# Optimization experiments

Hardware: AMD Instinct MI355X
Metric: run time of the kernel (lower is better)

Reference implementation:

```python
import jax, jax.numpy as jnp
import numpy as np

NEG_SLOPE = 0.01  # torch nn.LeakyReLU default


def _lrelu(x):
    return jax.nn.leaky_relu(x, NEG_SLOPE)


def _conv1x1(x, w):
    # x: [B,C,H,W], w: [O,C] -> [B,O,H,W]  (1x1 conv, no bias)
    return jnp.einsum('bchw,oc->bohw', x, w)


def _distance_matrix(scale, H, W, dtype):
    # even-scale branch of the torch code
    x = jnp.arange(-(scale // 2), scale // 2 + 1, dtype=dtype)  # len scale+1
    x = jnp.concatenate([x[: (scale + 1) // 2], x[(scale + 1) // 2 + 1:]])  # drop middle -> len scale
    d0 = jnp.broadcast_to(x[None, :], (scale, scale))
    d1 = d0.T
    d2 = jnp.sqrt(d0 ** 2 + d1 ** 2)
    dm = jnp.stack([d0, d1, d2], axis=0)            # [3, s, s]
    dm = jnp.tile(dm, (1, H // scale, W // scale))   # [3, H, W]
    return dm[None]                                  # [1, 3, H, W]


def setup_inputs() -> dict:
    key = jax.random.key(0)
    ks = jax.random.split(key, 10)
    B, C, h, w, scale = 1, 16, 256, 256, 4
    H, W = h * scale, w * scale
    f32 = jnp.float32

    def kaiming(k, shape):
        fan_out = shape[0]
        std = np.sqrt(2.0 / fan_out)
        return (jax.random.normal(k, shape, dtype=f32) * std)

    return {
        'lr_feature': jax.random.normal(ks[0], (B, C, h, w), dtype=f32),
        'hr_feature': jax.random.normal(ks[1], (B, C, H, W), dtype=f32),
        'w0': kaiming(ks[2], (32, 64)),
        'w1': kaiming(ks[3], (16, 32)),
        'w2': kaiming(ks[4], (8, 16)),
        'w3': kaiming(ks[5], (1, 8)),
        's0': kaiming(ks[6], (3, 3)),
        's1': kaiming(ks[7], (2, 3)),
        's2': kaiming(ks[8], (1, 2)),
        'wf': jnp.abs(kaiming(ks[9], (1, 2))),
    }


def reference(lr_feature, hr_feature, w0, w1, w2, w3, s0, s1, s2, wf):
    B, C, h, w = lr_feature.shape
    H, W = hr_feature.shape[-2:]
    scale = W // w  # static under jit

    # nearest-neighbor expand of lr_feature to hr resolution
    lr_up = jnp.repeat(jnp.repeat(lr_feature, scale, axis=2), scale, axis=3)

    # representation: [B, 4C, H, W]
    rep = jnp.concatenate(
        [lr_up, hr_feature, lr_up * hr_feature, (lr_up - hr_feature) ** 2], axis=1)

    # similarity_measure1: 4C->32->16->8->1, leaky relu after each
    o = _lrelu(_conv1x1(rep, w0))
    o = _lrelu(_conv1x1(o, w1))
    o = _lrelu(_conv1x1(o, w2))
    weights1 = _lrelu(_conv1x1(o, w3))  # [B,1,H,W]

    # similarity_measure2 on the tiled distance matrix: 3->3->2->1
    dm = _distance_matrix(scale, H, W, lr_feature.dtype)  # [1,3,H,W]
    o2 = _lrelu(_conv1x1(dm, s0))
    o2 = _lrelu(_conv1x1(o2, s1))
    weights2 = _lrelu(_conv1x1(o2, s2))  # [1,1,H,W]

    # fuse with abs-constrained weights
    fused_in = jnp.concatenate([weights1, weights2], axis=1)  # [B,2,H,W] (B=1)
    mapping = _lrelu(_conv1x1(fused_in, jnp.abs(wf)))
    return mapping
```

## Files before the change

### kernel.cpp

```cpp
#include <hip/hip_runtime.h>
#include <hip/hip_bf16.h>


typedef __attribute__((ext_vector_type(8))) short bf16x8;
typedef __attribute__((ext_vector_type(4))) short s16x4;
typedef __attribute__((ext_vector_type(4))) float f32x4;

union B8 { bf16x8 v; short2 p[4]; int d[4]; };
union B4 { s16x4 v; short2 p[2]; int d[2]; };

__device__ __forceinline__ float lrelu(float x) { return fmaxf(x, 0.01f * x); }

__device__ __forceinline__ short2 cvt2(float a, float b) {
    __hip_bfloat162 h = __float22bfloat162_rn(make_float2(a, b));
    short2 s; __builtin_memcpy(&s, &h, 4); return s;
}

__global__ __launch_bounds__(256) void ctx_mfma(
    const float* __restrict__ lr,  const float* __restrict__ hr,
    const float* __restrict__ w0g, const float* __restrict__ w1g,
    const float* __restrict__ w2g, const float* __restrict__ w3g,
    const float* __restrict__ s0g, const float* __restrict__ s1g,
    const float* __restrict__ s2g, const float* __restrict__ wfg,
    float* __restrict__ out)
{
    constexpr int W = 1024, HW = 1024 * 1024, LHW = 256 * 256;

    const int tid  = threadIdx.x;
    const int lane = tid & 63;
    const int g    = lane >> 4;
    const int px   = lane & 15;

    const int wave_id = blockIdx.x * 4 + (tid >> 6);
    const int y  = wave_id >> 3;
    const int xw = (wave_id & 7) << 7;

    B8 a1[2][2];
    #pragma unroll
    for (int m = 0; m < 2; ++m)
        #pragma unroll
        for (int q = 0; q < 2; ++q) {
            const float* wp = w0g + (m * 16 + px) * 64 + q * 32 + g * 8;
            #pragma unroll
            for (int j = 0; j < 4; ++j) a1[m][q].p[j] = cvt2(wp[2 * j], wp[2 * j + 1]);
        }
    B8 a2;
    {
        const float* wp = w1g + px * 32 + g * 8;
        #pragma unroll
        for (int j = 0; j < 4; ++j) a2.p[j] = cvt2(wp[2 * j], wp[2 * j + 1]);
    }
    B8 a3;
    {
        const bool val = (px < 8) && (g < 2);
        const float* wp = w2g + (px & 7) * 16 + (g & 1) * 8;
        const short2 z2s = make_short2(0, 0);
        #pragma unroll
        for (int j = 0; j < 4; ++j) a3.p[j] = val ? cvt2(wp[2 * j], wp[2 * j + 1]) : z2s;
    }
    const float4 w3v = *(const float4*)(w3g + (g & 1) * 4);

    const int xi = px & 3, yi = y & 3;
    const float d0 = (float)xi + ((xi < 2) ? -2.f : -1.f);
    const float d1 = (float)yi + ((yi < 2) ? -2.f : -1.f);
    const float d2 = sqrtf(d0 * d0 + d1 * d1);
    const float q0 = lrelu(s0g[0] * d0 + s0g[1] * d1 + s0g[2] * d2);
    const float q1 = lrelu(s0g[3] * d0 + s0g[4] * d1 + s0g[5] * d2);
    const float q2 = lrelu(s0g[6] * d0 + s0g[7] * d1 + s0g[8] * d2);
    const float u0 = lrelu(s1g[0] * q0 + s1g[1] * q1 + s1g[2] * q2);
    const float u1 = lrelu(s1g[3] * q0 + s1g[4] * q1 + s1g[5] * q2);
    const float wt2 = lrelu(s2g[0] * u0 + s2g[1] * u1);
    const float awf0 = fabsf(wfg[0]), awf1 = fabsf(wfg[1]);

    const int s0l = px + 16 * ((2 * g) & 3);
    const int s1l = s0l + 16;
    const bool glo = (g < 2);

    const int cb = (g & 1) << 3;
    int hr_idx[8], lr_idx[8];
    #pragma unroll
    for (int j = 0; j < 8; ++j) {
        hr_idx[j] = (cb + j) * HW  + y * W + xw + px;
        lr_idx[j] = (cb + j) * LHW + (y >> 2) * 256 + (xw >> 2) + (px >> 2);
    }
    const int oidx = y * W + xw + px;
    const f32x4 zf = {0.f, 0.f, 0.f, 0.f};

#define LOADT(LV, HV, T)                                                      \
    {                                                                         \
        _Pragma("unroll")                                                     \
        for (int j = 0; j < 8; ++j) {                                         \
            HV[j] = hr[hr_idx[j] + (T) * 16];                                 \
            LV[j] = lr[lr_idx[j] + (T) * 4];                                  \
        }                                                                     \
    }

#define COMPUTE(LV, HV, T)                                                    \
    {                                                                         \
        B8 b0, b1;                                                            \
        _Pragma("unroll")                                                     \
        for (int j = 0; j < 4; ++j) {                                         \
            float ua = glo ? LV[2 * j]     : HV[2 * j];                       \
            float ub = glo ? LV[2 * j + 1] : HV[2 * j + 1];                   \
            b0.p[j] = cvt2(ua, ub);                                           \
            float da = LV[2 * j]     - HV[2 * j];                             \
            float db = LV[2 * j + 1] - HV[2 * j + 1];                         \
            float pa = glo ? LV[2 * j]     * HV[2 * j]     : da * da;         \
            float pb = glo ? LV[2 * j + 1] * HV[2 * j + 1] : db * db;         \
            b1.p[j] = cvt2(pa, pb);                                           \
        }                                                                     \
        f32x4 acc1a = __builtin_amdgcn_mfma_f32_16x16x32_bf16(a1[0][0].v, b0.v, zf, 0, 0, 0); \
        acc1a = __builtin_amdgcn_mfma_f32_16x16x32_bf16(a1[0][1].v, b1.v, acc1a, 0, 0, 0);    \
        f32x4 acc1b = __builtin_amdgcn_mfma_f32_16x16x32_bf16(a1[1][0].v, b0.v, zf, 0, 0, 0); \
        acc1b = __builtin_amdgcn_mfma_f32_16x16x32_bf16(a1[1][1].v, b1.v, acc1b, 0, 0, 0);    \
        B4 za, zq;                                                            \
        za.p[0] = cvt2(lrelu(acc1a.x), lrelu(acc1a.y));                       \
        za.p[1] = cvt2(lrelu(acc1a.z), lrelu(acc1a.w));                       \
        zq.p[0] = cvt2(lrelu(acc1b.x), lrelu(acc1b.y));                       \
        zq.p[1] = cvt2(lrelu(acc1b.z), lrelu(acc1b.w));                       \
                   \
        int A0 = __shfl(za.d[0], s0l, 64);                                    \
        int A1 = __shfl(za.d[1], s0l, 64);                                    \
        int A2 = __shfl(za.d[0], s1l, 64);                                    \
        int A3 = __shfl(za.d[1], s1l, 64);                                    \
        int Q0 = __shfl(zq.d[0], s0l, 64);                                    \
        int Q1 = __shfl(zq.d[1], s0l, 64);                                    \
        int Q2 = __shfl(zq.d[0], s1l, 64);                                    \
        int Q3 = __shfl(zq.d[1], s1l, 64);                                    \
        B8 b2;                                                                \
        b2.d[0] = glo ? A0 : Q0;                                              \
        b2.d[1] = glo ? A1 : Q1;                                              \
        b2.d[2] = glo ? A2 : Q2;                                              \
        b2.d[3] = glo ? A3 : Q3;                                              \
        f32x4 acc2 = __builtin_amdgcn_mfma_f32_16x16x32_bf16(a2.v, b2.v, zf, 0, 0, 0); \
        B4 z2q;                                                               \
        z2q.p[0] = cvt2(lrelu(acc2.x), lrelu(acc2.y));                        \
        z2q.p[1] = cvt2(lrelu(acc2.z), lrelu(acc2.w));                        \
               \
        B8 b3;                                                                \
        b3.d[0] = __shfl(z2q.d[0], s0l, 64);                                  \
        b3.d[1] = __shfl(z2q.d[1], s0l, 64);                                  \
        b3.d[2] = __shfl(z2q.d[0], s1l, 64);                                  \
        b3.d[3] = __shfl(z2q.d[1], s1l, 64);                                  \
        f32x4 acc3 = __builtin_amdgcn_mfma_f32_16x16x32_bf16(a3.v, b3.v, zf, 0, 0, 0); \
        float part = w3v.x * lrelu(acc3.x) + w3v.y * lrelu(acc3.y)            \
                   + w3v.z * lrelu(acc3.z) + w3v.w * lrelu(acc3.w);           \
        float sum = part + __shfl_xor(part, 16, 64);                          \
        float wt1 = lrelu(sum);                                               \
        float res = lrelu(awf0 * wt1 + awf1 * wt2);                           \
        if (g == 0) out[oidx + (T) * 16] = res;                               \
    }

    float la[8], ha[8], lb[8], hb[8];
    LOADT(la, ha, 0);
    #pragma unroll
    for (int tt = 0; tt < 8; tt += 2) {
        LOADT(lb, hb, tt + 1);
        COMPUTE(la, ha, tt);
        if (tt + 2 < 8) LOADT(la, ha, tt + 2);
        COMPUTE(lb, hb, tt + 1);
    }
#undef LOADT
#undef COMPUTE
}

extern "C" void kernel_launch(void* const* d_in, const int* in_sizes, int n_in,
                              void* d_out, int out_size, void* d_ws, size_t ws_size,
                              hipStream_t stream) {
    const float* lr = (const float*)d_in[0];
    const float* hr = (const float*)d_in[1];
    const float* w0 = (const float*)d_in[2];
    const float* w1 = (const float*)d_in[3];
    const float* w2 = (const float*)d_in[4];
    const float* w3 = (const float*)d_in[5];
    const float* s0 = (const float*)d_in[6];
    const float* s1 = (const float*)d_in[7];
    const float* s2 = (const float*)d_in[8];
    const float* wf = (const float*)d_in[9];
    float* o = (float*)d_out;

    ctx_mfma<<<2048, 256, 0, stream>>>(lr, hr, w0, w1, w2, w3, s0, s1, s2, wf, o);
}
```

Baseline: 139.4 us.

## Stage inputs via direct global-to-LDS loads with triple-buffered pipeline

Each wave now copies its hr and lr input tiles straight into per-wave LDS with 16-byte global_load_lds transfers. These copies are triple-buffered and paced by manual vmcnt waits, instead of using per-lane scalar register loads with double buffering. The aim is to keep more memory requests in flight and issue wider loads for this latency-limited streaming kernel. The cost is extra LDS reads per tile, plus reliance on hand-counted vmcnt values that must match the issued load count exactly.

```diff
diff --git a/kernel.cpp b/kernel.cpp
--- a/kernel.cpp
+++ b/kernel.cpp
@@ -16,6 +16,12 @@
     short2 s; __builtin_memcpy(&s, &h, 4); return s;
 }
 
+__device__ __forceinline__ void gl16(const float* g, float* l) {
+    __builtin_amdgcn_global_load_lds(
+        (const __attribute__((address_space(1))) void*)g,
+        (__attribute__((address_space(3))) void*)l, 16, 0, 0);
+}
+
 __global__ __launch_bounds__(256) void ctx_mfma(
     const float* __restrict__ lr,  const float* __restrict__ hr,
     const float* __restrict__ w0g, const float* __restrict__ w1g,
@@ -26,12 +32,16 @@
 {
     constexpr int W = 1024, HW = 1024 * 1024, LHW = 256 * 256;
 
+    __shared__ __align__(16) float shr[4][3][16][16];
+    __shared__ __align__(16) float slr[4][3][16][4];
+
     const int tid  = threadIdx.x;
     const int lane = tid & 63;
+    const int widx = tid >> 6;
     const int g    = lane >> 4;
     const int px   = lane & 15;
 
-    const int wave_id = blockIdx.x * 4 + (tid >> 6);
+    const int wave_id = blockIdx.x * 4 + widx;
     const int y  = wave_id >> 3;
     const int xw = (wave_id & 7) << 7;
 
@@ -75,38 +85,38 @@
     const int s0l = px + 16 * ((2 * g) & 3);
     const int s1l = s0l + 16;
     const bool glo = (g < 2);
+    const int cb = (g & 1) << 3;
 
-    const int cb = (g & 1) << 3;
-    int hr_idx[8], lr_idx[8];
-    #pragma unroll
-    for (int j = 0; j < 8; ++j) {
-        hr_idx[j] = (cb + j) * HW  + y * W + xw + px;
-        lr_idx[j] = (cb + j) * LHW + (y >> 2) * 256 + (xw >> 2) + (px >> 2);
-    }
+    const float* hrs = hr + (lane >> 2) * HW + y * W + xw + (lane & 3) * 4;
+    const float* lrs = lr + (lane & 15) * LHW + (y >> 2) * 256 + (xw >> 2);
+
     const int oidx = y * W + xw + px;
     const f32x4 zf = {0.f, 0.f, 0.f, 0.f};
 
-#define LOADT(LV, HV, T)                                                      \
+#define STAGE(BUF, T)                                                         \
     {                                                                         \
+        gl16(hrs + (T) * 16, &shr[widx][BUF][0][0]);                          \
+        if (lane < 16) gl16(lrs + (T) * 4, &slr[widx][BUF][0][0]);            \
+    }
+
+#define COMP(BUF, T)                                                          \
+    {                                                                         \
+        float lrv[8], hrv[8];                                                 \
         _Pragma("unroll")                                                     \
         for (int j = 0; j < 8; ++j) {                                         \
-            HV[j] = hr[hr_idx[j] + (T) * 16];                                 \
-            LV[j] = lr[lr_idx[j] + (T) * 4];                                  \
+            hrv[j] = shr[widx][BUF][cb + j][px];                              \
+            lrv[j] = slr[widx][BUF][cb + j][px >> 2];                         \
         }                                                                     \
-    }
-
-#define COMPUTE(LV, HV, T)                                                    \
-    {                                                                         \
         B8 b0, b1;                                                            \
         _Pragma("unroll")                                                     \
         for (int j = 0; j < 4; ++j) {                                         \
-            float ua = glo ? LV[2 * j]     : HV[2 * j];                       \
-            float ub = glo ? LV[2 * j + 1] : HV[2 * j + 1];                   \
+            float ua = glo ? lrv[2 * j]     : hrv[2 * j];                     \
+            float ub = glo ? lrv[2 * j + 1] : hrv[2 * j + 1];                 \
             b0.p[j] = cvt2(ua, ub);                                           \
-            float da = LV[2 * j]     - HV[2 * j];                             \
-            float db = LV[2 * j + 1] - HV[2 * j + 1];                         \
-            float pa = glo ? LV[2 * j]     * HV[2 * j]     : da * da;         \
-            float pb = glo ? LV[2 * j + 1] * HV[2 * j + 1] : db * db;         \
+            float da = lrv[2 * j]     - hrv[2 * j];                           \
+            float db = lrv[2 * j + 1] - hrv[2 * j + 1];                       \
+            float pa = glo ? lrv[2 * j]     * hrv[2 * j]     : da * da;       \
+            float pb = glo ? lrv[2 * j + 1] * hrv[2 * j + 1] : db * db;       \
             b1.p[j] = cvt2(pa, pb);                                           \
         }                                                                     \
         f32x4 acc1a = __builtin_amdgcn_mfma_f32_16x16x32_bf16(a1[0][0].v, b0.v, zf, 0, 0, 0); \
@@ -118,7 +128,6 @@
         za.p[1] = cvt2(lrelu(acc1a.z), lrelu(acc1a.w));                       \
         zq.p[0] = cvt2(lrelu(acc1b.x), lrelu(acc1b.y));                       \
         zq.p[1] = cvt2(lrelu(acc1b.z), lrelu(acc1b.w));                       \
-                   \
         int A0 = __shfl(za.d[0], s0l, 64);                                    \
         int A1 = __shfl(za.d[1], s0l, 64);                                    \
         int A2 = __shfl(za.d[0], s1l, 64);                                    \
@@ -136,7 +145,6 @@
         B4 z2q;                                                               \
         z2q.p[0] = cvt2(lrelu(acc2.x), lrelu(acc2.y));                        \
         z2q.p[1] = cvt2(lrelu(acc2.z), lrelu(acc2.w));                        \
-               \
         B8 b3;                                                                \
         b3.d[0] = __shfl(z2q.d[0], s0l, 64);                                  \
         b3.d[1] = __shfl(z2q.d[1], s0l, 64);                                  \
@@ -151,17 +159,22 @@
         if (g == 0) out[oidx + (T) * 16] = res;                               \
     }
 
-    float la[8], ha[8], lb[8], hb[8];
-    LOADT(la, ha, 0);
-    #pragma unroll
-    for (int tt = 0; tt < 8; tt += 2) {
-        LOADT(lb, hb, tt + 1);
-        COMPUTE(la, ha, tt);
-        if (tt + 2 < 8) LOADT(la, ha, tt + 2);
-        COMPUTE(lb, hb, tt + 1);
-    }
-#undef LOADT
-#undef COMPUTE
+#define WAITV(N) asm volatile("s_waitcnt vmcnt(" #N ")" ::: "memory")
+
+    STAGE(0, 0)
+    STAGE(1, 1)
+    STAGE(2, 2) WAITV(4); COMP(0, 0)
+    STAGE(0, 3) WAITV(5); COMP(1, 1)
+    STAGE(1, 4) WAITV(6); COMP(2, 2)
+    STAGE(2, 5) WAITV(6); COMP(0, 3)
+    STAGE(0, 6) WAITV(6); COMP(1, 4)
+    STAGE(1, 7) WAITV(6); COMP(2, 5)
+    WAITV(4); COMP(0, 6)
+    WAITV(2); COMP(1, 7)
+
+#undef STAGE
+#undef COMP
+#undef WAITV
 }
 
 extern "C" void kernel_launch(void* const* d_in, const int* in_sizes, int n_in,
```

New measurement: 141.4 us. Within noise of the previous version (+1.4%).
